# Optimization experiments

Measured on AMD Instinct MI355X. Metric: run time of the kernel, lower is better.

## Reference

```python
import jax, jax.numpy as jnp
import numpy as np

N, D, K, O, DEGREE = 524288, 64, 64, 32, 6


def setup_inputs() -> dict:
    key = jax.random.key(0)
    kz, kT, kC, kb = jax.random.split(key, 4)
    z = jax.random.normal(kz, (N, D), dtype=jnp.float32)
    T = jax.random.normal(kT, (DEGREE, K, D), dtype=jnp.float32)  # T[i-1] == T_i
    C = jax.random.normal(kC, (O, K), dtype=jnp.float32)
    beta = jax.random.normal(kb, (O,), dtype=jnp.float32)
    return {"z": z, "T": T, "C": C, "beta": beta}


def reference(z, T, C, beta):
    degree = T.shape[0]
    k = T.shape[1]
    z = z.reshape(-1, T.shape[2])  # [N, d]
    # P0 = ones(k) (buffer T0), P1 = z @ T1.T (T1 is NOT row-normalized)
    p_prev = jnp.ones((k,), dtype=z.dtype)          # P_{i-2}
    p_curr = jnp.matmul(z, T[0].T)                  # P_{i-1}, [N, k]
    for i in range(2, degree + 1):
        Ti = T[i - 1]
        Ti = Ti / jnp.sum(Ti, axis=1, keepdims=True)  # row-normalize for i >= 2
        coef = (2.0 * i - 1.0) / i
        p_new = jnp.matmul(z, coef * Ti.T) * p_curr - ((i - 1.0) / i) * p_prev
        p_prev, p_curr = p_curr, p_new
    return jnp.matmul(p_curr, C.T) + beta  # [N, o]
```

## Files before the change

kernel.cpp:

```cpp
#include <hip/hip_runtime.h>


typedef _Float16 f16x8 __attribute__((ext_vector_type(8)));
typedef __fp16   h16x2 __attribute__((ext_vector_type(2)));
typedef short    s16x8 __attribute__((ext_vector_type(8)));
typedef float    f32x4 __attribute__((ext_vector_type(4)));
typedef float    f32x2 __attribute__((ext_vector_type(2)));
struct f32x2p { f32x2 lo, hi; };

#define NN      524288
#define BLOCKS  256
#define THREADS 512
#define NWAVES  8
#define NITER   4

#define BH_OFF    0
#define CF_OFF    49152
#define SCALE_OFF 53248
#define SCR_OFF   54784
#define SMEM_BYTES (SCR_OFF + NWAVES * 4096)

__device__ __forceinline__ unsigned short f2bf(float x) {
    unsigned u = __builtin_bit_cast(unsigned, x);
    return (unsigned short)((u + 0x7FFFu + ((u >> 16) & 1u)) >> 16);
}

__global__ __launch_bounds__(THREADS) void leg_mfma(
    const float* __restrict__ z, const float* __restrict__ T,
    const float* __restrict__ Cm, const float* __restrict__ beta,
    float* __restrict__ out)
{
    extern __shared__ char smem[];
    float* scale_s = (float*)(smem + SCALE_OFF);
    const int tid  = (int)threadIdx.x;
    const int lane = tid & 63;
    const int wv   = tid >> 6;
    const int lrow = lane & 15;
    const int lhi  = lane >> 4;

    if (tid < 384) {
        const int mat = tid >> 6, kc = tid & 63;
        const float4* tr = (const float4*)(T + (size_t)((mat << 6) + kc) * 64);
        float s = 0.f;
        #pragma unroll
        for (int q = 0; q < 16; ++q) { float4 v = tr[q]; s += v.x + v.y + v.z + v.w; }
        const float smul[6] = {1.f, 3.f, 1.25f, 28.f / 9.f, 81.f / 64.f, 704.f / 225.f};
        const float sc = (mat == 0) ? 1.f : smul[mat] / s;
        scale_s[tid] = sc;
    }
    __syncthreads();

    for (int g = tid; g < 3072; g += THREADS) {
        const int mat = g >> 9;
        const int s   = (g >> 8) & 1;
        const int f   = (g >> 6) & 3;
        const int l   = g & 63;
        const int kc  = (l & 15) + (f << 4);
        const int d0  = ((l >> 4) << 3) + (s << 5);
        const float sc = scale_s[(mat << 6) + kc];
        const float* src = T + (size_t)((mat << 6) + kc) * 64 + d0;
        const float4 v0 = *(const float4*)(src);
        const float4 v1 = *(const float4*)(src + 4);
        const float vv[8] = {v0.x, v0.y, v0.z, v0.w, v1.x, v1.y, v1.z, v1.w};
        f16x8 hi;
        #pragma unroll
        for (int j = 0; j < 8; ++j) hi[j] = (_Float16)(vv[j] * sc);
        const int fr = (((mat << 1) + s) << 2) + f;
        *(f16x8*)(smem + BH_OFF + fr * 1024 + l * 16) = hi;
    }
    if (tid < 256) {
        const int s  = (tid >> 7) & 1;
        const int fo = (tid >> 6) & 1;
        const int l  = tid & 63;
        const int o  = (l & 15) + (fo << 4);
        const int k0 = ((l >> 4) << 3) + (s << 5);
        const float* src = Cm + (size_t)o * 64 + k0;
        const float4 v0 = *(const float4*)src;
        const float4 v1 = *(const float4*)(src + 4);
        const float vv[8] = {v0.x, v0.y, v0.z, v0.w, v1.x, v1.y, v1.z, v1.w};
        s16x8 fr;
        #pragma unroll
        for (int j = 0; j < 8; ++j) fr[j] = (short)f2bf(vv[j] * 0.3125f);
        *(s16x8*)(smem + CF_OFF + ((s << 1) + fo) * 1024 + l * 16) = fr;
    }
    __syncthreads();

    const int    gw      = blockIdx.x * NWAVES + wv;
    const size_t rowbase = (size_t)gw * 256;
    float* scr = (float*)(smem + SCR_OFF + wv * 4096);

    const float beta0 = beta[lrow];
    const float beta1 = beta[16 + lrow];
    const f32x2 one2 = {1.f, 1.f};

    f16x8 zh[2][2][2];

    auto leg_step = [&](int mat, f32x4 (&PC)[2][2][4], f32x4 (&PT)[2][2][4]) {
        __builtin_amdgcn_s_setprio(1);
        #pragma unroll
        for (int f = 0; f < 4; ++f) {
            const int fr0 = mat * 8 + f;
            const int fr1 = mat * 8 + 4 + f;
            const f16x8 bh0 = *(const f16x8*)(smem + BH_OFF + fr0 * 1024 + lane * 16);
            const f16x8 bh1 = *(const f16x8*)(smem + BH_OFF + fr1 * 1024 + lane * 16);
            #pragma unroll
            for (int u = 0; u < 2; ++u)
                #pragma unroll
                for (int t = 0; t < 2; ++t) {
                    f32x4 a = {0.f, 0.f, 0.f, 0.f};
                    a = __builtin_amdgcn_mfma_f32_16x16x32_f16(zh[u][t][0], bh0, a, 0, 0, 0);
                    a = __builtin_amdgcn_mfma_f32_16x16x32_f16(zh[u][t][1], bh1, a, 0, 0, 0);
                    f32x2p av = __builtin_bit_cast(f32x2p, a);
                    f32x2p pc = __builtin_bit_cast(f32x2p, PC[u][t][f]);
                    f32x2p pt = __builtin_bit_cast(f32x2p, PT[u][t][f]);
                    pt.lo = av.lo * pc.lo - pt.lo;
                    pt.hi = av.hi * pc.hi - pt.hi;
                    PT[u][t][f] = __builtin_bit_cast(f32x4, pt);
                }
        }
        __builtin_amdgcn_s_setprio(0);
    };

    for (int it = 0; it < NITER; ++it) {
        #pragma unroll
        for (int u = 0; u < 2; ++u)
            #pragma unroll
            for (int t = 0; t < 2; ++t)
                #pragma unroll
                for (int s = 0; s < 2; ++s) {
                    const float* p = z + (rowbase + (size_t)it * 64 + u * 32 + t * 16 + lrow) * 64
                                       + (s << 5) + (lhi << 3);
                    const float4 q0 = *(const float4*)(p);
                    const float4 q1 = *(const float4*)(p + 4);
                    union { f16x8 v; h16x2 h[4]; } uz;
                    uz.h[0] = __builtin_amdgcn_cvt_pkrtz(q0.x, q0.y);
                    uz.h[1] = __builtin_amdgcn_cvt_pkrtz(q0.z, q0.w);
                    uz.h[2] = __builtin_amdgcn_cvt_pkrtz(q1.x, q1.y);
                    uz.h[3] = __builtin_amdgcn_cvt_pkrtz(q1.z, q1.w);
                    zh[u][t][s] = uz.v;
                }

        f32x4 pA[2][2][4], pB[2][2][4];
        __builtin_amdgcn_s_setprio(1);
        #pragma unroll
        for (int f = 0; f < 4; ++f) {
            const int fr0 = f, fr1 = 4 + f;
            const f16x8 bh0 = *(const f16x8*)(smem + BH_OFF + fr0 * 1024 + lane * 16);
            const f16x8 bh1 = *(const f16x8*)(smem + BH_OFF + fr1 * 1024 + lane * 16);
            #pragma unroll
            for (int u = 0; u < 2; ++u)
                #pragma unroll
                for (int t = 0; t < 2; ++t) {
                    f32x4 a = {0.f, 0.f, 0.f, 0.f};
                    a = __builtin_amdgcn_mfma_f32_16x16x32_f16(zh[u][t][0], bh0, a, 0, 0, 0);
                    a = __builtin_amdgcn_mfma_f32_16x16x32_f16(zh[u][t][1], bh1, a, 0, 0, 0);
                    pA[u][t][f] = a;
                }
        }
        #pragma unroll
        for (int f = 0; f < 4; ++f) {
            const int fr0 = 8 + f, fr1 = 12 + f;
            const f16x8 bh0 = *(const f16x8*)(smem + BH_OFF + fr0 * 1024 + lane * 16);
            const f16x8 bh1 = *(const f16x8*)(smem + BH_OFF + fr1 * 1024 + lane * 16);
            #pragma unroll
            for (int u = 0; u < 2; ++u)
                #pragma unroll
                for (int t = 0; t < 2; ++t) {
                    f32x4 a = {0.f, 0.f, 0.f, 0.f};
                    a = __builtin_amdgcn_mfma_f32_16x16x32_f16(zh[u][t][0], bh0, a, 0, 0, 0);
                    a = __builtin_amdgcn_mfma_f32_16x16x32_f16(zh[u][t][1], bh1, a, 0, 0, 0);
                    f32x2p av = __builtin_bit_cast(f32x2p, a);
                    f32x2p pa = __builtin_bit_cast(f32x2p, pA[u][t][f]);
                    f32x2p pb;
                    pb.lo = av.lo * pa.lo - one2;
                    pb.hi = av.hi * pa.hi - one2;
                    pB[u][t][f] = __builtin_bit_cast(f32x4, pb);
                }
        }
        __builtin_amdgcn_s_setprio(0);
        leg_step(2, pB, pA);
        leg_step(3, pA, pB);
        leg_step(4, pB, pA);
        leg_step(5, pA, pB);

        s16x8 ch[2][2];
        #pragma unroll
        for (int s = 0; s < 2; ++s)
            #pragma unroll
            for (int fo = 0; fo < 2; ++fo)
                ch[s][fo] = *(const s16x8*)(smem + CF_OFF + ((s << 1) + fo) * 1024 + lane * 16);
        #pragma unroll
        for (int u = 0; u < 2; ++u)
            #pragma unroll
            for (int t = 0; t < 2; ++t) {
                #pragma unroll
                for (int f = 0; f < 4; ++f)
                    #pragma unroll
                    for (int r = 0; r < 4; ++r) {
                        const int row = lhi * 4 + r;
                        const int k   = (f << 4) + lrow;
                        const int g4  = (k >> 2) ^ row;
                        scr[row * 64 + g4 * 4 + (k & 3)] = pB[u][t][f][r];
                    }
                s16x8 p6h[2];
                #pragma unroll
                for (int s = 0; s < 2; ++s) {
                    const int g0 = lhi * 2 + s * 8;
                    const float4 q0 = *(const float4*)(scr + lrow * 64 + ((g0)     ^ lrow) * 4);
                    const float4 q1 = *(const float4*)(scr + lrow * 64 + ((g0 + 1) ^ lrow) * 4);
                    const float vv[8] = {q0.x, q0.y, q0.z, q0.w, q1.x, q1.y, q1.z, q1.w};
                    union { s16x8 v; unsigned w[4]; } ph;
                    #pragma unroll
                    for (int m = 0; m < 4; ++m)
                        asm("v_cvt_pk_bf16_f32 %0, %1, %2"
                            : "=v"(ph.w[m]) : "v"(vv[2 * m]), "v"(vv[2 * m + 1]));
                    p6h[s] = ph.v;
                }
                #pragma unroll
                for (int fo = 0; fo < 2; ++fo) {
                    f32x4 o = {0.f, 0.f, 0.f, 0.f};
                    o = __builtin_amdgcn_mfma_f32_16x16x32_bf16(p6h[0], ch[0][fo], o, 0, 0, 0);
                    o = __builtin_amdgcn_mfma_f32_16x16x32_bf16(p6h[1], ch[1][fo], o, 0, 0, 0);
                    const float bb = fo ? beta1 : beta0;
                    const size_t r0 = rowbase + (size_t)it * 64 + u * 32 + t * 16 + lhi * 4;
                    #pragma unroll
                    for (int r = 0; r < 4; ++r)
                        out[(r0 + r) * 32 + (fo << 4) + lrow] = o[r] + bb;
                }
            }
    }
}

extern "C" void kernel_launch(void* const* d_in, const int* in_sizes, int n_in,
                              void* d_out, int out_size, void* d_ws, size_t ws_size,
                              hipStream_t stream) {
    const float* z    = (const float*)d_in[0];
    const float* T    = (const float*)d_in[1];
    const float* C    = (const float*)d_in[2];
    const float* beta = (const float*)d_in[3];
    float* out = (float*)d_out;
    (void)in_sizes; (void)n_in; (void)out_size; (void)d_ws; (void)ws_size;

    hipFuncSetAttribute((const void*)leg_mfma,
                        hipFuncAttributeMaxDynamicSharedMemorySize, SMEM_BYTES);
    leg_mfma<<<BLOCKS, THREADS, SMEM_BYTES, stream>>>(z, T, C, beta, out);
}
```

Measured before the change: 48.48 us.

## Double grid to 512 blocks, shrink LDS to 64KB static, keep C fragments in registers

```diff
diff --git a/kernel.cpp b/kernel.cpp
--- a/kernel.cpp
+++ b/kernel.cpp
@@ -9,16 +9,13 @@
 struct f32x2p { f32x2 lo, hi; };
 
 #define NN      524288
-#define BLOCKS  256
+#define BLOCKS  512
 #define THREADS 512
 #define NWAVES  8
-#define NITER   4
-
-#define BH_OFF    0
-#define CF_OFF    49152
-#define SCALE_OFF 53248
-#define SCR_OFF   54784
-#define SMEM_BYTES (SCR_OFF + NWAVES * 4096)
+#define NITER   2
+
+#define BH_OFF  0
+#define SCR_OFF 49152
 
 __device__ __forceinline__ unsigned short f2bf(float x) {
     unsigned u = __builtin_bit_cast(unsigned, x);
@@ -30,13 +27,29 @@
     const float* __restrict__ Cm, const float* __restrict__ beta,
     float* __restrict__ out)
 {
-    extern __shared__ char smem[];
-    float* scale_s = (float*)(smem + SCALE_OFF);
+    __shared__ char smem[65536];
+    float* scale_s = (float*)(smem + SCR_OFF);
     const int tid  = (int)threadIdx.x;
     const int lane = tid & 63;
     const int wv   = tid >> 6;
     const int lrow = lane & 15;
     const int lhi  = lane >> 4;
+
+    s16x8 ch[2][2];
+    #pragma unroll
+    for (int s = 0; s < 2; ++s)
+        #pragma unroll
+        for (int fo = 0; fo < 2; ++fo) {
+            const int o  = lrow + (fo << 4);
+            const int k0 = (lhi << 3) + (s << 5);
+            const float4 v0 = *(const float4*)(Cm + (size_t)o * 64 + k0);
+            const float4 v1 = *(const float4*)(Cm + (size_t)o * 64 + k0 + 4);
+            const float vv[8] = {v0.x, v0.y, v0.z, v0.w, v1.x, v1.y, v1.z, v1.w};
+            s16x8 fr;
+            #pragma unroll
+            for (int j = 0; j < 8; ++j) fr[j] = (short)f2bf(vv[j] * 0.3125f);
+            ch[s][fo] = fr;
+        }
 
     if (tid < 384) {
         const int mat = tid >> 6, kc = tid & 63;
@@ -68,26 +81,11 @@
         const int fr = (((mat << 1) + s) << 2) + f;
         *(f16x8*)(smem + BH_OFF + fr * 1024 + l * 16) = hi;
     }
-    if (tid < 256) {
-        const int s  = (tid >> 7) & 1;
-        const int fo = (tid >> 6) & 1;
-        const int l  = tid & 63;
-        const int o  = (l & 15) + (fo << 4);
-        const int k0 = ((l >> 4) << 3) + (s << 5);
-        const float* src = Cm + (size_t)o * 64 + k0;
-        const float4 v0 = *(const float4*)src;
-        const float4 v1 = *(const float4*)(src + 4);
-        const float vv[8] = {v0.x, v0.y, v0.z, v0.w, v1.x, v1.y, v1.z, v1.w};
-        s16x8 fr;
-        #pragma unroll
-        for (int j = 0; j < 8; ++j) fr[j] = (short)f2bf(vv[j] * 0.3125f);
-        *(s16x8*)(smem + CF_OFF + ((s << 1) + fo) * 1024 + l * 16) = fr;
-    }
     __syncthreads();
 
     const int    gw      = blockIdx.x * NWAVES + wv;
-    const size_t rowbase = (size_t)gw * 256;
-    float* scr = (float*)(smem + SCR_OFF + wv * 4096);
+    const size_t rowbase = (size_t)gw * 128;
+    float* scr = (float*)(smem + SCR_OFF) + wv * 512;
 
     const float beta0 = beta[lrow];
     const float beta1 = beta[16 + lrow];
@@ -183,32 +181,32 @@
         leg_step(4, pB, pA);
         leg_step(5, pA, pB);
 
-        s16x8 ch[2][2];
-        #pragma unroll
-        for (int s = 0; s < 2; ++s)
-            #pragma unroll
-            for (int fo = 0; fo < 2; ++fo)
-                ch[s][fo] = *(const s16x8*)(smem + CF_OFF + ((s << 1) + fo) * 1024 + lane * 16);
         #pragma unroll
         for (int u = 0; u < 2; ++u)
             #pragma unroll
             for (int t = 0; t < 2; ++t) {
-                #pragma unroll
-                for (int f = 0; f < 4; ++f)
-                    #pragma unroll
-                    for (int r = 0; r < 4; ++r) {
-                        const int row = lhi * 4 + r;
-                        const int k   = (f << 4) + lrow;
-                        const int g4  = (k >> 2) ^ row;
-                        scr[row * 64 + g4 * 4 + (k & 3)] = pB[u][t][f][r];
+                s16x8 p6h[2];
+                #pragma unroll
+                for (int s = 0; s < 2; ++s) {
+                    #pragma unroll
+                    for (int f_ = 0; f_ < 2; ++f_) {
+                        const int f    = 2 * s + f_;
+                        const int colp = (f_ << 4) + lrow;
+                        #pragma unroll
+                        for (int r = 0; r < 4; ++r) {
+                            const int row = lhi * 4 + r;
+                            const int g4  = ((colp >> 2) ^ row) & 7;
+                            scr[row * 32 + g4 * 4 + (colp & 3)] = pB[u][t][f][r];
+                        }
                     }
-                s16x8 p6h[2];
-                #pragma unroll
-                for (int s = 0; s < 2; ++s) {
-                    const int g0 = lhi * 2 + s * 8;
-                    const float4 q0 = *(const float4*)(scr + lrow * 64 + ((g0)     ^ lrow) * 4);
-                    const float4 q1 = *(const float4*)(scr + lrow * 64 + ((g0 + 1) ^ lrow) * 4);
-                    const float vv[8] = {q0.x, q0.y, q0.z, q0.w, q1.x, q1.y, q1.z, q1.w};
+                    float vv[8];
+                    #pragma unroll
+                    for (int jg = 0; jg < 2; ++jg) {
+                        const int g4r = (((lhi << 1) + jg) ^ lrow) & 7;
+                        const float4 q = *(const float4*)(scr + lrow * 32 + g4r * 4);
+                        vv[jg * 4 + 0] = q.x; vv[jg * 4 + 1] = q.y;
+                        vv[jg * 4 + 2] = q.z; vv[jg * 4 + 3] = q.w;
+                    }
                     union { s16x8 v; unsigned w[4]; } ph;
                     #pragma unroll
                     for (int m = 0; m < 4; ++m)
@@ -241,7 +239,5 @@
     float* out = (float*)d_out;
     (void)in_sizes; (void)n_in; (void)out_size; (void)d_ws; (void)ws_size;
 
-    hipFuncSetAttribute((const void*)leg_mfma,
-                        hipFuncAttributeMaxDynamicSharedMemorySize, SMEM_BYTES);
-    leg_mfma<<<BLOCKS, THREADS, SMEM_BYTES, stream>>>(z, T, C, beta, out);
+    leg_mfma<<<BLOCKS, THREADS, 0, stream>>>(z, T, C, beta, out);
 }
```

Measured after the change: 58.74 us. +21.2%, slower.
